# Performance work log

Measured on AMD Instinct MI355X. Metric: run time of the kernel, lower is better.

Reference implementation:

```python
import jax, jax.numpy as jnp
import numpy as np

NUM_LOCAL_EXPERTS = 8
D_MODEL = 1024
D_FF = 4096
B, EC = 4, NUM_LOCAL_EXPERTS * 1024  # dim1 = E * capacity


def setup_inputs() -> dict:
    key = jax.random.key(0)
    k_in, k_w1, k_w2 = jax.random.split(key, 3)
    s1 = 1.0 / np.sqrt(D_MODEL)
    s2 = 1.0 / np.sqrt(D_FF)
    return {
        "inputs": jax.random.normal(k_in, (B, EC, D_MODEL), dtype=jnp.float32),
        # torch.nn.Linear stores weight as [out, in]; one stack per local expert
        "w1": jax.random.normal(k_w1, (NUM_LOCAL_EXPERTS, D_FF, D_MODEL), dtype=jnp.float32) * s1,
        "b1": jnp.zeros((NUM_LOCAL_EXPERTS, D_FF), dtype=jnp.float32),
        "w2": jax.random.normal(k_w2, (NUM_LOCAL_EXPERTS, D_MODEL, D_FF), dtype=jnp.float32) * s2,
        "b2": jnp.zeros((NUM_LOCAL_EXPERTS, D_MODEL), dtype=jnp.float32),
    }


def reference(inputs, w1, b1, w2, b2):
    # chunk(dim=1) into E equal pieces == reshape [B, E, C, D]; per-expert FFN
    # is then a single grouped GEMM over the expert axis; concat == reshape back.
    B_, EC_, D = inputs.shape
    E = w1.shape[0]
    C = EC_ // E
    x = inputs.reshape(B_, E, C, D)                       # [B, E, C, D]
    h = jnp.einsum('becd,efd->becf', x, w1) + b1[None, :, None, :]   # [B, E, C, F]
    h = jax.nn.gelu(h, approximate=False)
    y = jnp.einsum('becf,edf->becd', h, w2) + b2[None, :, None, :]   # [B, E, C, D]
    return y.reshape(B_, EC_, D)
```

## Files before the change

kernel.cpp:

```cpp
#include <hip/hip_runtime.h>
#include <cstdint>
#include <cstddef>


typedef __bf16 bf16;
typedef __attribute__((ext_vector_type(8))) __bf16 bf16x8;
typedef __attribute__((ext_vector_type(4))) __bf16 bf16x4;
typedef __attribute__((ext_vector_type(4))) float floatx4;

#define FENCE() asm volatile("" ::: "memory")
#define BAR() do { FENCE(); __builtin_amdgcn_s_barrier(); FENCE(); } while (0)
#define VMCNT4() asm volatile("s_waitcnt vmcnt(4)" ::: "memory")
#define VMCNT0() asm volatile("s_waitcnt vmcnt(0)" ::: "memory")
#define MFMA16(a, b, c) __builtin_amdgcn_mfma_f32_16x16x32_bf16((a), (b), (c), 0, 0, 0)

__device__ __forceinline__ void async_copy16(void* lds_ptr, const void* g_ptr) {
  __builtin_amdgcn_global_load_lds(
      (const __attribute__((address_space(1))) uint32_t*)g_ptr,
      (__attribute__((address_space(3))) uint32_t*)lds_ptr,
      16, 0, 0);
}

__global__ __launch_bounds__(256) void cvt_f32_to_bf16(
    const float4* __restrict__ src, bf16x4* __restrict__ dst, int n4) {
  int i = blockIdx.x * 256 + threadIdx.x;
  if (i < n4) {
    float4 v = src[i];
    bf16x4 o = {(bf16)v.x, (bf16)v.y, (bf16)v.z, (bf16)v.w};
    dst[i] = o;
  }
}

template <int KDIM, int NDIM, bool GELU, typename OutT>
__global__ __launch_bounds__(512, 2) void gemm256_8ph(
    const bf16* __restrict__ A,
    const bf16* __restrict__ Bw,
    const float* __restrict__ bias,
    OutT* __restrict__ Out) {
  constexpr int NT = KDIM / 64;
  constexpr int NB = NDIM / 256;
  constexpr int NWG = (32768 / 256) * NB;

  __shared__ bf16x8 ldsA[4096];
  __shared__ bf16x8 ldsB[4096];

  const int wgid = ((int)blockIdx.x & 7) * (NWG / 8) + ((int)blockIdx.x >> 3);
  const int n_blk = wgid % NB;
  const int m_blk = wgid / NB;
  const int e = (m_blk >> 2) & 7;

  const int tid = threadIdx.x;
  const int lane = tid & 63;
  const int wid = tid >> 6;
  const int wm = wid >> 2;
  const int wn = wid & 3;
  const int lo16 = lane & 15;
  const int q = lane >> 4;

  const bf16* Ab = A + (size_t)m_blk * 256 * KDIM;
  const bf16* Bb = Bw + (size_t)e * NDIM * KDIM + (size_t)n_blk * 256 * KDIM;

  const int srow = tid >> 3;
  const int skoff = ((tid & 7) ^ (srow & 7)) * 8;

  const int sl0 = q ^ (lo16 & 7);
  const int sl1 = (4 + q) ^ (lo16 & 7);
  const int aoff = wm * 1024 + lo16 * 8;
  const int boff = wn * 512 + lo16 * 8;

  floatx4 acc[8][4];
#pragma unroll
  for (int i = 0; i < 8; ++i)
#pragma unroll
    for (int j = 0; j < 4; ++j) acc[i][j] = (floatx4)(0.0f);

  bf16x8 afr[4][2];
  bf16x8 bfr[4][2];

#define STAGE_A(buf, h, kt_) do {                                              \
    const bf16* s_ = Ab + (size_t)((h) * 128 + srow) * KDIM + ((kt_)*64 + skoff); \
    bf16x8* d_ = &ldsA[((buf)*2 + (h)) * 1024 + tid];                          \
    async_copy16(d_, s_);                                                      \
    async_copy16(d_ + 512, s_ + (size_t)64 * KDIM);                            \
  } while (0)
#define STAGE_B(buf, h, kt_) do {                                              \
    const bf16* s_ = Bb + (size_t)((h) * 128 + srow) * KDIM + ((kt_)*64 + skoff); \
    bf16x8* d_ = &ldsB[((buf)*2 + (h)) * 1024 + tid];                          \
    async_copy16(d_, s_);                                                      \
    async_copy16(d_ + 512, s_ + (size_t)64 * KDIM);                            \
  } while (0)

  STAGE_B(0, 0, 0); STAGE_B(0, 1, 0);
  STAGE_A(0, 0, 0); STAGE_A(0, 1, 0);
  STAGE_B(1, 0, 1); STAGE_B(1, 1, 1);
  VMCNT4();
  BAR();

  for (int kt = 0; kt < NT; ++kt) {
    const int b = kt & 1;
    const int abase = b * 2048 + aoff;
    const int bbase = b * 2048 + boff;
    const int kA1 = (kt + 1 < NT) ? kt + 1 : NT - 1;
    const int kB2 = (kt + 2 < NT) ? kt + 2 : NT - 1;

#pragma unroll
    for (int i = 0; i < 4; ++i) {
      afr[i][0] = ldsA[abase + i * 128 + sl0];
      afr[i][1] = ldsA[abase + i * 128 + sl1];
    }
#pragma unroll
    for (int j = 0; j < 2; ++j) {
      bfr[j][0] = ldsB[bbase + j * 128 + sl0];
      bfr[j][1] = ldsB[bbase + j * 128 + sl1];
    }
    STAGE_A(b ^ 1, 0, kA1);
    BAR();
    __builtin_amdgcn_s_setprio(1);
#pragma unroll
    for (int i = 0; i < 4; ++i)
#pragma unroll
      for (int j = 0; j < 2; ++j) {
        acc[i][j] = MFMA16(afr[i][0], bfr[j][0], acc[i][j]);
        acc[i][j] = MFMA16(afr[i][1], bfr[j][1], acc[i][j]);
      }
    __builtin_amdgcn_s_setprio(0);
    BAR();

#pragma unroll
    for (int j = 2; j < 4; ++j) {
      bfr[j][0] = ldsB[bbase + j * 128 + sl0];
      bfr[j][1] = ldsB[bbase + j * 128 + sl1];
    }
    STAGE_A(b ^ 1, 1, kA1);
    BAR();
    __builtin_amdgcn_s_setprio(1);
#pragma unroll
    for (int i = 0; i < 4; ++i)
#pragma unroll
      for (int j = 2; j < 4; ++j) {
        acc[i][j] = MFMA16(afr[i][0], bfr[j][0], acc[i][j]);
        acc[i][j] = MFMA16(afr[i][1], bfr[j][1], acc[i][j]);
      }
    __builtin_amdgcn_s_setprio(0);
    BAR();

#pragma unroll
    for (int i = 0; i < 4; ++i) {
      afr[i][0] = ldsA[abase + 512 + i * 128 + sl0];
      afr[i][1] = ldsA[abase + 512 + i * 128 + sl1];
    }
    STAGE_B(b, 0, kB2);
    BAR();
    __builtin_amdgcn_s_setprio(1);
#pragma unroll
    for (int i = 0; i < 4; ++i)
#pragma unroll
      for (int j = 0; j < 2; ++j) {
        acc[4 + i][j] = MFMA16(afr[i][0], bfr[j][0], acc[4 + i][j]);
        acc[4 + i][j] = MFMA16(afr[i][1], bfr[j][1], acc[4 + i][j]);
      }
    __builtin_amdgcn_s_setprio(0);
    BAR();

    STAGE_B(b, 1, kB2);
    BAR();
    __builtin_amdgcn_s_setprio(1);
#pragma unroll
    for (int i = 0; i < 4; ++i)
#pragma unroll
      for (int j = 2; j < 4; ++j) {
        acc[4 + i][j] = MFMA16(afr[i][0], bfr[j][0], acc[4 + i][j]);
        acc[4 + i][j] = MFMA16(afr[i][1], bfr[j][1], acc[4 + i][j]);
      }
    __builtin_amdgcn_s_setprio(0);
    VMCNT4();
    BAR();
  }
  VMCNT0();

  const float* be = bias + e * NDIM;
  const size_t row0 = (size_t)m_blk * 256 + (size_t)wm * 128 + q * 4;
  const int col0 = n_blk * 256 + wn * 64 + lo16;
#pragma unroll
  for (int j = 0; j < 4; ++j) {
    const int col = col0 + j * 16;
    const float bv = be[col];
#pragma unroll
    for (int i = 0; i < 8; ++i) {
#pragma unroll
      for (int r = 0; r < 4; ++r) {
        const size_t row = row0 + i * 16 + r;
        float v = acc[i][j][r] + bv;
        if (GELU) v = 0.5f * v * (1.0f + erff(v * 0.70710678118654752f));
        __builtin_nontemporal_store((OutT)v, &Out[row * (size_t)NDIM + col]);
      }
    }
  }
#undef STAGE_A
#undef STAGE_B
}

extern "C" void kernel_launch(void* const* d_in, const int* in_sizes, int n_in,
                              void* d_out, int out_size, void* d_ws, size_t ws_size,
                              hipStream_t stream) {
  const float* x  = (const float*)d_in[0];
  const float* w1 = (const float*)d_in[1];
  const float* b1 = (const float*)d_in[2];
  const float* w2 = (const float*)d_in[3];
  const float* b2 = (const float*)d_in[4];
  float* out = (float*)d_out;
  char* ws = (char*)d_ws;

  bf16* xb  = (bf16*)(ws + 0);
  bf16* w1b = (bf16*)(ws + 67108864ull);
  bf16* w2b = (bf16*)(ws + 134217728ull);
  bf16* hb  = (bf16*)(ws + 201326592ull);

  const int n4 = 33554432 / 4;
  dim3 cgrid(n4 / 256), cblk(256);
  cvt_f32_to_bf16<<<cgrid, cblk, 0, stream>>>((const float4*)x,  (bf16x4*)xb,  n4);
  cvt_f32_to_bf16<<<cgrid, cblk, 0, stream>>>((const float4*)w1, (bf16x4*)w1b, n4);
  cvt_f32_to_bf16<<<cgrid, cblk, 0, stream>>>((const float4*)w2, (bf16x4*)w2b, n4);

  gemm256_8ph<1024, 4096, true, bf16>
      <<<dim3(2048), dim3(512), 0, stream>>>(xb, w1b, b1, hb);
  gemm256_8ph<4096, 1024, false, float>
      <<<dim3(512), dim3(512), 0, stream>>>(hb, w2b, b2, out);
}
```

Before: 1.182 ms.

## Triple-buffer A tiles for two-tile prefetch and use polynomial erf GELU

Expands LDS for the A operand to three buffers, so A is prefetched two k-tiles ahead like B. The prologue stages two tiles of both operands and the wait count is raised to vmcnt(8). This is meant to hide more global-load latency. It also replaces erff in the GELU epilogue with an Abramowitz-Stegun polynomial using a fast exp and divide, which cuts epilogue math at the cost of a small accuracy loss. The extra LDS (about 160KB per block) may no longer fit two workgroups per CU and so could reduce occupancy.

```diff
diff --git a/kernel.cpp b/kernel.cpp
--- a/kernel.cpp
+++ b/kernel.cpp
@@ -10,8 +10,7 @@
 
 #define FENCE() asm volatile("" ::: "memory")
 #define BAR() do { FENCE(); __builtin_amdgcn_s_barrier(); FENCE(); } while (0)
-#define VMCNT4() asm volatile("s_waitcnt vmcnt(4)" ::: "memory")
-#define VMCNT0() asm volatile("s_waitcnt vmcnt(0)" ::: "memory")
+#define VMCNT(n) asm volatile("s_waitcnt vmcnt(" #n ")" ::: "memory")
 #define MFMA16(a, b, c) __builtin_amdgcn_mfma_f32_16x16x32_bf16((a), (b), (c), 0, 0, 0)
 
 __device__ __forceinline__ void async_copy16(void* lds_ptr, const void* g_ptr) {
@@ -19,6 +18,19 @@
       (const __attribute__((address_space(1))) uint32_t*)g_ptr,
       (__attribute__((address_space(3))) uint32_t*)lds_ptr,
       16, 0, 0);
+}
+
+__device__ __forceinline__ float gelu_fast(float x) {
+  const float ax = fabsf(x);
+  const float az = ax * 0.70710678118654752f;
+  const float t = __fdividef(1.0f, fmaf(az, 0.3275911f, 1.0f));
+  const float e = __expf(-az * az);
+  float p = fmaf(t, 1.061405429f, -1.453152027f);
+  p = fmaf(t, p, 1.421413741f);
+  p = fmaf(t, p, -0.284496736f);
+  p = fmaf(t, p, 0.254829592f);
+  const float erf_abs = fmaf(-(p * t), e, 1.0f);
+  return 0.5f * (x + ax * erf_abs);
 }
 
 __global__ __launch_bounds__(256) void cvt_f32_to_bf16(
@@ -41,7 +53,7 @@
   constexpr int NB = NDIM / 256;
   constexpr int NWG = (32768 / 256) * NB;
 
-  __shared__ bf16x8 ldsA[4096];
+  __shared__ bf16x8 ldsA[6144];
   __shared__ bf16x8 ldsB[4096];
 
   const int wgid = ((int)blockIdx.x & 7) * (NWG / 8) + ((int)blockIdx.x >> 3);
@@ -79,30 +91,31 @@
 
 #define STAGE_A(buf, h, kt_) do {                                              \
     const bf16* s_ = Ab + (size_t)((h) * 128 + srow) * KDIM + ((kt_)*64 + skoff); \
-    bf16x8* d_ = &ldsA[((buf)*2 + (h)) * 1024 + tid];                          \
+    bf16x8* d_ = &ldsA[(buf) * 2048 + (h) * 1024 + tid];                       \
     async_copy16(d_, s_);                                                      \
     async_copy16(d_ + 512, s_ + (size_t)64 * KDIM);                            \
   } while (0)
 #define STAGE_B(buf, h, kt_) do {                                              \
     const bf16* s_ = Bb + (size_t)((h) * 128 + srow) * KDIM + ((kt_)*64 + skoff); \
-    bf16x8* d_ = &ldsB[((buf)*2 + (h)) * 1024 + tid];                          \
+    bf16x8* d_ = &ldsB[(buf) * 2048 + (h) * 1024 + tid];                       \
     async_copy16(d_, s_);                                                      \
     async_copy16(d_ + 512, s_ + (size_t)64 * KDIM);                            \
   } while (0)
 
+  STAGE_A(0, 0, 0); STAGE_A(0, 1, 0);
   STAGE_B(0, 0, 0); STAGE_B(0, 1, 0);
-  STAGE_A(0, 0, 0); STAGE_A(0, 1, 0);
+  STAGE_A(1, 0, 1); STAGE_A(1, 1, 1);
   STAGE_B(1, 0, 1); STAGE_B(1, 1, 1);
-  VMCNT4();
+  VMCNT(8);
   BAR();
 
+  int ar = 0;
+  int as = 2;
   for (int kt = 0; kt < NT; ++kt) {
-    const int b = kt & 1;
-    const int abase = b * 2048 + aoff;
-    const int bbase = b * 2048 + boff;
-    const int kA1 = (kt + 1 < NT) ? kt + 1 : NT - 1;
-    const int kB2 = (kt + 2 < NT) ? kt + 2 : NT - 1;
-
+    const int bb = kt & 1;
+    const int abase = ar * 2048 + aoff;
+    const int bbase = bb * 2048 + boff;
+    const int kN = (kt + 2 < NT) ? kt + 2 : NT - 1;
 #pragma unroll
     for (int i = 0; i < 4; ++i) {
       afr[i][0] = ldsA[abase + i * 128 + sl0];
@@ -113,7 +126,7 @@
       bfr[j][0] = ldsB[bbase + j * 128 + sl0];
       bfr[j][1] = ldsB[bbase + j * 128 + sl1];
     }
-    STAGE_A(b ^ 1, 0, kA1);
+    STAGE_A(as, 0, kN);
     BAR();
     __builtin_amdgcn_s_setprio(1);
 #pragma unroll
@@ -131,7 +144,7 @@
       bfr[j][0] = ldsB[bbase + j * 128 + sl0];
       bfr[j][1] = ldsB[bbase + j * 128 + sl1];
     }
-    STAGE_A(b ^ 1, 1, kA1);
+    STAGE_A(as, 1, kN);
     BAR();
     __builtin_amdgcn_s_setprio(1);
 #pragma unroll
@@ -149,7 +162,7 @@
       afr[i][0] = ldsA[abase + 512 + i * 128 + sl0];
       afr[i][1] = ldsA[abase + 512 + i * 128 + sl1];
     }
-    STAGE_B(b, 0, kB2);
+    STAGE_B(bb, 0, kN);
     BAR();
     __builtin_amdgcn_s_setprio(1);
 #pragma unroll
@@ -162,7 +175,7 @@
     __builtin_amdgcn_s_setprio(0);
     BAR();
 
-    STAGE_B(b, 1, kB2);
+    STAGE_B(bb, 1, kN);
     BAR();
     __builtin_amdgcn_s_setprio(1);
 #pragma unroll
@@ -173,10 +186,13 @@
         acc[4 + i][j] = MFMA16(afr[i][1], bfr[j][1], acc[4 + i][j]);
       }
     __builtin_amdgcn_s_setprio(0);
-    VMCNT4();
-    BAR();
+    VMCNT(8);
+    BAR();
+
+    ar = (ar == 2) ? 0 : ar + 1;
+    as = (as == 2) ? 0 : as + 1;
   }
-  VMCNT0();
+  VMCNT(0);
 
   const float* be = bias + e * NDIM;
   const size_t row0 = (size_t)m_blk * 256 + (size_t)wm * 128 + q * 4;
@@ -191,7 +207,7 @@
       for (int r = 0; r < 4; ++r) {
         const size_t row = row0 + i * 16 + r;
         float v = acc[i][j][r] + bv;
-        if (GELU) v = 0.5f * v * (1.0f + erff(v * 0.70710678118654752f));
+        if (GELU) v = gelu_fast(v);
         __builtin_nontemporal_store((OutT)v, &Out[row * (size_t)NDIM + col]);
       }
     }
```

Measured after the change: 1.182 ms. No clear change (+0.0%).
